# Optimization experiments

Measured on AMD Instinct MI355X. Metric: run time of the kernel, lower is better.

Reference implementation:

```python
import jax, jax.numpy as jnp
import numpy as np

HIDDEN = 2048
NUM_HEADS = 16
HEAD_DIM = HIDDEN // NUM_HEADS  # 128
SCALE = HEAD_DIM ** -0.5


def setup_inputs() -> dict:
    key = jax.random.key(0)
    ks = jax.random.split(key, 5)
    B, S = 2, 2048
    init = HIDDEN ** -0.5  # roughly kaiming-uniform scale for Linear weights
    return {
        "hidden_states": jax.random.normal(ks[0], (B, S, HIDDEN), dtype=jnp.float32),
        "Wq": jax.random.normal(ks[1], (HIDDEN, HIDDEN), dtype=jnp.float32) * init,
        "Wk": jax.random.normal(ks[2], (HIDDEN, HIDDEN), dtype=jnp.float32) * init,
        "Wv": jax.random.normal(ks[3], (HIDDEN, HIDDEN), dtype=jnp.float32) * init,
        "Wo": jax.random.normal(ks[4], (HIDDEN, HIDDEN), dtype=jnp.float32) * init,
    }


def reference(hidden_states, Wq, Wk, Wv, Wo):
    B, S, _ = hidden_states.shape
    # Projections (nn.Linear: x @ W.T; weights stored as [out, in])
    q = (hidden_states @ Wq.T).reshape(B, S, NUM_HEADS, HEAD_DIM).transpose(0, 2, 1, 3)
    k = (hidden_states @ Wk.T).reshape(B, S, NUM_HEADS, HEAD_DIM).transpose(0, 2, 1, 3)
    v = (hidden_states @ Wv.T).reshape(B, S, NUM_HEADS, HEAD_DIM).transpose(0, 2, 1, 3)
    # Full quadratic attention (faithful to the source's explicit materialization)
    scores = jnp.einsum("bhqd,bhkd->bhqk", q, k) * SCALE  # [B,H,S,S]
    probs = jax.nn.softmax(scores, axis=-1)
    attn = jnp.einsum("bhqk,bhkd->bhqd", probs, v)  # [B,H,S,Dh]
    attn = attn.transpose(0, 2, 1, 3).reshape(B, S, HIDDEN)
    return attn @ Wo.T
```

## Files before the change

### kernel.cpp

```cpp
#include <hip/hip_runtime.h>
#include <cstdint>

#define HIDDEN 2048
#define NHEADS 16
#define DH 128
#define BATCH 2
#define SEQ 2048
#define MTOT 4096
#define BH (BATCH * NHEADS)

typedef __attribute__((ext_vector_type(8))) short bf16x8;
typedef __attribute__((ext_vector_type(4))) float f32x4;

static constexpr float QSCALE = (float)(0.08838834764831845 * 1.4426950408889634);

__device__ __forceinline__ unsigned short f2bf(float f) {
  union { float f; uint32_t u; } v; v.f = f;
  uint32_t r = v.u + 0x7FFFu + ((v.u >> 16) & 1u);
  return (unsigned short)(r >> 16);
}
__device__ __forceinline__ uint32_t cvtpk(float lo, float hi) {
  uint32_t r;
  asm("v_cvt_pk_bf16_f32 %0, %1, %2" : "=v"(r) : "v"(lo), "v"(hi));
  return r;
}
__device__ __forceinline__ f32x4 mfma16(bf16x8 a, bf16x8 b, f32x4 c) {
  return __builtin_amdgcn_mfma_f32_16x16x32_bf16(a, b, c, 0, 0, 0);
}

typedef const __attribute__((address_space(1))) unsigned char* gas1_t;
typedef __attribute__((address_space(3))) unsigned char* las3_t;
__device__ __forceinline__ void gll16(const void* g, void* l) {
  __builtin_amdgcn_global_load_lds((gas1_t)g, (las3_t)l, 16, 0, 0);
}

__global__ __launch_bounds__(256) void cast_all(
    const float* __restrict__ X, const float* __restrict__ Wq,
    const float* __restrict__ Wk, const float* __restrict__ Wv,
    const float* __restrict__ Wo, unsigned short* __restrict__ Xb,
    unsigned short* __restrict__ Wqb, unsigned short* __restrict__ Wkb,
    unsigned short* __restrict__ Wvb, unsigned short* __restrict__ Wob) {
  const int n1 = MTOT * HIDDEN;
  const int i = (blockIdx.x * 256 + threadIdx.x) * 4;
  const float* s;
  unsigned short* d;
  int o;
  if (i < n1) {
    s = X; d = Xb; o = i;
  } else {
    const int j = i - n1;
    const int w = j >> 22;
    o = j & ((1 << 22) - 1);
    s = (w == 0) ? Wq : (w == 1) ? Wk : (w == 2) ? Wv : Wo;
    d = (w == 0) ? Wqb : (w == 1) ? Wkb : (w == 2) ? Wvb : Wob;
  }
  float4 f = *(const float4*)&s[o];
  ushort4 u;
  u.x = f2bf(f.x); u.y = f2bf(f.y); u.z = f2bf(f.z); u.w = f2bf(f.w);
  *(ushort4*)&d[o] = u;
}

__global__ __launch_bounds__(256) void gemm_qkv_pipe(
    const unsigned short* __restrict__ A, const unsigned short* __restrict__ Wq,
    const unsigned short* __restrict__ Wk, const unsigned short* __restrict__ Wv,
    unsigned short* __restrict__ Qb, unsigned short* __restrict__ Kb,
    unsigned short* __restrict__ Vb) {
  __shared__ __align__(16) char SM[65536];
  const int tid = threadIdx.x;
  const int lane = tid & 63, wv = tid >> 6;
  const int wr = wv >> 1, wc = wv & 1;
  const int g = lane >> 4, lr = lane & 15;
  const int which = blockIdx.x >> 4;
  const int m0 = blockIdx.y * 128, n0 = (blockIdx.x & 15) * 128;
  const unsigned short* W = (which == 0) ? Wq : (which == 1) ? Wk : Wv;

  const unsigned short* aS[4];
  const unsigned short* bS[4];
#pragma unroll
  for (int j = 0; j < 4; ++j) {
    const int c = j * 256 + tid;
    const int row = c >> 3, cc = (c & 7) ^ (row & 7);
    aS[j] = A + (size_t)(m0 + row) * HIDDEN + cc * 8;
    bS[j] = W + (size_t)(n0 + row) * HIDDEN + cc * 8;
  }

  f32x4 acc[4][4];
#pragma unroll
  for (int i = 0; i < 4; ++i)
#pragma unroll
    for (int j = 0; j < 4; ++j) acc[i][j] = (f32x4){0.f, 0.f, 0.f, 0.f};

#pragma unroll
  for (int j = 0; j < 4; ++j) {
    gll16(aS[j], SM + j * 4096 + wv * 1024);
    gll16(bS[j], SM + 16384 + j * 4096 + wv * 1024);
  }

  const int rx = lr & 7;
  for (int t = 0; t < 32; ++t) {
    const char* slot = SM + (t & 1) * 32768;
    asm volatile("s_waitcnt vmcnt(0)" ::: "memory");
    __builtin_amdgcn_s_barrier();
    if (t + 1 < 32) {
      char* nslot = SM + ((t + 1) & 1) * 32768;
      const size_t ko = (size_t)(t + 1) * 64;
#pragma unroll
      for (int j = 0; j < 4; ++j) {
        gll16(aS[j] + ko, nslot + j * 4096 + wv * 1024);
        gll16(bS[j] + ko, nslot + 16384 + j * 4096 + wv * 1024);
      }
    }
    bf16x8 a0[4], b0[4], a1[4], b1[4];
#pragma unroll
    for (int mi = 0; mi < 4; ++mi) {
      const int row = wr * 64 + mi * 16 + lr;
      a0[mi] = *(const bf16x8*)(slot + row * 128 + ((g ^ rx) * 16));
      a1[mi] = *(const bf16x8*)(slot + row * 128 + (((4 + g) ^ rx) * 16));
    }
#pragma unroll
    for (int ni = 0; ni < 4; ++ni) {
      const int row = wc * 64 + ni * 16 + lr;
      b0[ni] = *(const bf16x8*)(slot + 16384 + row * 128 + ((g ^ rx) * 16));
      b1[ni] = *(const bf16x8*)(slot + 16384 + row * 128 + (((4 + g) ^ rx) * 16));
    }
    __builtin_amdgcn_s_setprio(1);
#pragma unroll
    for (int mi = 0; mi < 4; ++mi)
#pragma unroll
      for (int ni = 0; ni < 4; ++ni)
        acc[mi][ni] = mfma16(a0[mi], b0[ni], acc[mi][ni]);
#pragma unroll
    for (int mi = 0; mi < 4; ++mi)
#pragma unroll
      for (int ni = 0; ni < 4; ++ni)
        acc[mi][ni] = mfma16(a1[mi], b1[ni], acc[mi][ni]);
    __builtin_amdgcn_s_setprio(0);
  }

  const float alpha = (which == 0) ? QSCALE : 1.0f;
  unsigned short* C = (which == 0) ? Qb : (which == 1) ? Kb : Vb;
#pragma unroll
  for (int mi = 0; mi < 4; ++mi)
#pragma unroll
    for (int ni = 0; ni < 4; ++ni)
#pragma unroll
      for (int r = 0; r < 4; ++r) {
        const int row = m0 + wr * 64 + mi * 16 + g * 4 + r;
        const int col = n0 + wc * 64 + ni * 16 + lr;
        const unsigned short v = f2bf(acc[mi][ni][r] * alpha);
        const int b = row >> 11, s = row & (SEQ - 1);
        const int h = col >> 7, d = col & (DH - 1);
        const size_t base = (size_t)(b * NHEADS + h) * SEQ * DH;
        if (which == 0)
          C[base + (size_t)s * DH + d] = v;
        else if (which == 1)
          C[base + (size_t)(s >> 5) * 4096 + (d >> 3) * 256 + (s & 31) * 8 + (d & 7)] = v;
        else
          C[base + (size_t)(s >> 3) * 1024 + d * 8 + (s & 7)] = v;
      }
}

template <int VM, bool PF>
__device__ __forceinline__ void pipe_body(
    int kt, char* SM, const unsigned short* aS0, const unsigned short* aS1,
    const unsigned short* bS0, const unsigned short* bS1,
    const unsigned short* bS2, const unsigned short* bS3, int wv, int wr,
    int wc, int g, int lr, f32x4 (&acc)[4][4]) {
  const char* Ac = SM + (kt % 3) * 49152;
  const char* Bc = Ac + 16384;
  char* slot2 = SM + ((kt + 2) % 3) * 49152;
  const size_t ko = (size_t)(kt + 2) * 64;
  const int rx = lr & 7;
  bf16x8 a0[4], b0[4], a1[4], b1[4];
#pragma unroll
  for (int mi = 0; mi < 4; ++mi)
    a0[mi] = *(const bf16x8*)(Ac + (wr * 64 + mi * 16 + lr) * 128 + ((g ^ rx) * 16));
#pragma unroll
  for (int ni = 0; ni < 4; ++ni)
    b0[ni] = *(const bf16x8*)(Bc + (wc * 64 + ni * 16 + lr) * 128 + ((g ^ rx) * 16));
  if (PF) {
    gll16(aS0 + ko, slot2 + wv * 2048);
    gll16(aS1 + ko, slot2 + wv * 2048 + 1024);
    gll16(bS0 + ko, slot2 + 16384 + wv * 4096);
    gll16(bS1 + ko, slot2 + 16384 + wv * 4096 + 1024);
    gll16(bS2 + ko, slot2 + 16384 + wv * 4096 + 2048);
    gll16(bS3 + ko, slot2 + 16384 + wv * 4096 + 3072);
  }
#pragma unroll
  for (int mi = 0; mi < 4; ++mi)
    a1[mi] = *(const bf16x8*)(Ac + (wr * 64 + mi * 16 + lr) * 128 + (((4 + g) ^ rx) * 16));
#pragma unroll
  for (int ni = 0; ni < 4; ++ni)
    b1[ni] = *(const bf16x8*)(Bc + (wc * 64 + ni * 16 + lr) * 128 + (((4 + g) ^ rx) * 16));
  __builtin_amdgcn_s_setprio(1);
#pragma unroll
  for (int mi = 0; mi < 4; ++mi)
#pragma unroll
    for (int ni = 0; ni < 4; ++ni)
      acc[mi][ni] = mfma16(a0[mi], b0[ni], acc[mi][ni]);
#pragma unroll
  for (int mi = 0; mi < 4; ++mi)
#pragma unroll
    for (int ni = 0; ni < 4; ++ni)
      acc[mi][ni] = mfma16(a1[mi], b1[ni], acc[mi][ni]);
  __builtin_amdgcn_s_setprio(0);
  if (VM == 6) asm volatile("s_waitcnt vmcnt(6)" ::: "memory");
  else if (VM == 0) asm volatile("s_waitcnt vmcnt(0)" ::: "memory");
  if (VM >= 0) __builtin_amdgcn_s_barrier();
}

__global__ __launch_bounds__(512) void gemm_out_pipe(
    const unsigned short* __restrict__ A, const unsigned short* __restrict__ W,
    float* __restrict__ C) {
  __shared__ __align__(16) char SM[147456];
  const int tid = threadIdx.x;
  const int lane = tid & 63, wv = tid >> 6;
  const int wr = wv >> 2, wc = wv & 3;
  const int g = lane >> 4, lr = lane & 15;
  const int m0 = blockIdx.y * 128, n0 = blockIdx.x * 256;

  const int idxA0 = wv * 128 + lane, idxA1 = idxA0 + 64;
  const int rA0 = idxA0 >> 3, cA0 = (idxA0 & 7) ^ (rA0 & 7);
  const int rA1 = idxA1 >> 3, cA1 = (idxA1 & 7) ^ (rA1 & 7);
  const unsigned short* aS0 = A + (size_t)(m0 + rA0) * HIDDEN + cA0 * 8;
  const unsigned short* aS1 = A + (size_t)(m0 + rA1) * HIDDEN + cA1 * 8;
  const int idxB0 = wv * 256 + lane, idxB1 = idxB0 + 64,
            idxB2 = idxB0 + 128, idxB3 = idxB0 + 192;
  const int rB0 = idxB0 >> 3, cB0 = (idxB0 & 7) ^ (rB0 & 7);
  const int rB1 = idxB1 >> 3, cB1 = (idxB1 & 7) ^ (rB1 & 7);
  const int rB2 = idxB2 >> 3, cB2 = (idxB2 & 7) ^ (rB2 & 7);
  const int rB3 = idxB3 >> 3, cB3 = (idxB3 & 7) ^ (rB3 & 7);
  const unsigned short* bS0 = W + (size_t)(n0 + rB0) * HIDDEN + cB0 * 8;
  const unsigned short* bS1 = W + (size_t)(n0 + rB1) * HIDDEN + cB1 * 8;
  const unsigned short* bS2 = W + (size_t)(n0 + rB2) * HIDDEN + cB2 * 8;
  const unsigned short* bS3 = W + (size_t)(n0 + rB3) * HIDDEN + cB3 * 8;

  f32x4 acc[4][4];
#pragma unroll
  for (int i = 0; i < 4; ++i)
#pragma unroll
    for (int j = 0; j < 4; ++j) acc[i][j] = (f32x4){0.f, 0.f, 0.f, 0.f};

#pragma unroll
  for (int tt = 0; tt < 2; ++tt) {
    char* slot = SM + tt * 49152;
    const size_t ko = (size_t)tt * 64;
    gll16(aS0 + ko, slot + wv * 2048);
    gll16(aS1 + ko, slot + wv * 2048 + 1024);
    gll16(bS0 + ko, slot + 16384 + wv * 4096);
    gll16(bS1 + ko, slot + 16384 + wv * 4096 + 1024);
    gll16(bS2 + ko, slot + 16384 + wv * 4096 + 2048);
    gll16(bS3 + ko, slot + 16384 + wv * 4096 + 3072);
  }
  asm volatile("s_waitcnt vmcnt(6)" ::: "memory");
  __builtin_amdgcn_s_barrier();

  for (int kt = 0; kt < 30; ++kt)
    pipe_body<6, true>(kt, SM, aS0, aS1, bS0, bS1, bS2, bS3, wv, wr, wc, g,
                       lr, acc);
  pipe_body<0, false>(30, SM, aS0, aS1, bS0, bS1, bS2, bS3, wv, wr, wc, g,
                      lr, acc);
  pipe_body<-1, false>(31, SM, aS0, aS1, bS0, bS1, bS2, bS3, wv, wr, wc, g,
                       lr, acc);

#pragma unroll
  for (int mi = 0; mi < 4; ++mi)
#pragma unroll
    for (int ni = 0; ni < 4; ++ni)
#pragma unroll
      for (int r = 0; r < 4; ++r) {
        const int row = m0 + wr * 64 + mi * 16 + g * 4 + r;
        const int col = n0 + wc * 64 + ni * 16 + lr;
        C[(size_t)row * HIDDEN + col] = acc[mi][ni][r];
      }
}

__global__ __launch_bounds__(256, 4) void attn_mfma(const unsigned short* __restrict__ Q,
                                                    const unsigned short* __restrict__ K,
                                                    const unsigned short* __restrict__ V,
                                                    unsigned short* __restrict__ Ab) {
  const int bid = blockIdx.x;
  const int bh = bid & 31;
  const int q0 = (bid >> 5) * 64;
  const int tid = threadIdx.x;
  const int wv = tid >> 6, lane = tid & 63;
  const int g = lane >> 4, lr = lane & 15;
  const unsigned short* Qh = Q + (size_t)bh * SEQ * DH;
  const unsigned short* Kh = K + (size_t)bh * SEQ * DH;
  const unsigned short* Vh = V + (size_t)bh * SEQ * DH;

  __shared__ __align__(16) unsigned short Kls[2][4096];
  __shared__ __align__(16) unsigned short Vls[2][4096];
  __shared__ __align__(16) unsigned short Pw[4][16][40];

  bf16x8 qf[4];
#pragma unroll
  for (int kb = 0; kb < 4; ++kb)
    qf[kb] = *(const bf16x8*)&Qh[(size_t)(q0 + wv * 16 + lr) * DH + kb * 32 + g * 8];

  f32x4 acc[8];
#pragma unroll
  for (int dn = 0; dn < 8; ++dn) acc[dn] = (f32x4){0.f, 0.f, 0.f, 0.f};
  float mrun = -1e30f;
  float lrun = 0.f;

#pragma unroll
  for (int j = 0; j < 2; ++j) {
    const int c = j * 256 + tid;
    gll16(Kh + (size_t)c * 8, (char*)&Kls[0][0] + j * 4096 + wv * 1024);
    gll16(Vh + (size_t)c * 8, (char*)&Vls[0][0] + j * 4096 + wv * 1024);
  }

  for (int t = 0; t < 64; ++t) {
    const int cur = t & 1;
    asm volatile("s_waitcnt vmcnt(0)" ::: "memory");
    __builtin_amdgcn_s_barrier();
    if (t + 1 < 64) {
      const unsigned short* Kn = Kh + (size_t)(t + 1) * 4096;
      const unsigned short* Vn = Vh + (size_t)(t + 1) * 4096;
      char* kd = (char*)&Kls[cur ^ 1][0];
      char* vd = (char*)&Vls[cur ^ 1][0];
#pragma unroll
      for (int j = 0; j < 2; ++j) {
        const int c = j * 256 + tid;
        gll16(Kn + (size_t)c * 8, kd + j * 4096 + wv * 1024);
        gll16(Vn + (size_t)c * 8, vd + j * 4096 + wv * 1024);
      }
    }

    const char* Kc = (const char*)&Kls[cur][0];
    const char* Vc = (const char*)&Vls[cur][0];

    f32x4 st0 = (f32x4){0.f, 0.f, 0.f, 0.f};
    f32x4 st1 = (f32x4){0.f, 0.f, 0.f, 0.f};
    __builtin_amdgcn_s_setprio(1);
#pragma unroll
    for (int kb = 0; kb < 4; ++kb) {
      const int cb = (kb * 4 + g) * 32;
      bf16x8 kf0 = *(const bf16x8*)(Kc + (cb + lr) * 16);
      bf16x8 kf1 = *(const bf16x8*)(Kc + (cb + 16 + lr) * 16);
      st0 = mfma16(kf0, qf[kb], st0);
      st1 = mfma16(kf1, qf[kb], st1);
    }
    __builtin_amdgcn_s_setprio(0);
    float mt = fmaxf(fmaxf(fmaxf(st0[0], st0[1]), fmaxf(st0[2], st0[3])),
                     fmaxf(fmaxf(st1[0], st1[1]), fmaxf(st1[2], st1[3])));
    mt = fmaxf(mt, __shfl_xor(mt, 16));
    mt = fmaxf(mt, __shfl_xor(mt, 32));
    if (!__all(mt <= mrun + 8.0f)) {
      const float mnew = fmaxf(mrun, mt);
      const float corr = __builtin_amdgcn_exp2f(mrun - mnew);
      lrun *= corr;
      mrun = mnew;
      const f32x4 cv = (f32x4){__shfl(corr, g * 4 + 0), __shfl(corr, g * 4 + 1),
                               __shfl(corr, g * 4 + 2), __shfl(corr, g * 4 + 3)};
#pragma unroll
      for (int dn = 0; dn < 8; ++dn) acc[dn] *= cv;
    }
    float p[8], ls = 0.f;
#pragma unroll
    for (int r = 0; r < 4; ++r) {
      p[r] = __builtin_amdgcn_exp2f(st0[r] - mrun);
      p[4 + r] = __builtin_amdgcn_exp2f(st1[r] - mrun);
      ls += p[r] + p[4 + r];
    }
    lrun += ls;
    uint2 pk0, pk1;
    pk0.x = cvtpk(p[0], p[1]); pk0.y = cvtpk(p[2], p[3]);
    pk1.x = cvtpk(p[4], p[5]); pk1.y = cvtpk(p[6], p[7]);
    *(uint2*)&Pw[wv][lr][4 * g] = pk0;
    *(uint2*)&Pw[wv][lr][16 + 4 * g] = pk1;
    bf16x8 ap = *(const bf16x8*)&Pw[wv][lr][8 * g];
    __builtin_amdgcn_s_setprio(1);
#pragma unroll
    for (int dn = 0; dn < 8; ++dn) {
      bf16x8 vf = *(const bf16x8*)(Vc + (g * 128 + dn * 16 + lr) * 16);
      acc[dn] = mfma16(ap, vf, acc[dn]);
    }
    __builtin_amdgcn_s_setprio(0);
  }

  const int b = bh >> 4, h = bh & 15;
  lrun += __shfl_xor(lrun, 16);
  lrun += __shfl_xor(lrun, 32);
  const float inv = 1.f / lrun;
  float ir[4];
#pragma unroll
  for (int r = 0; r < 4; ++r) ir[r] = __shfl(inv, g * 4 + r);
#pragma unroll
  for (int dn = 0; dn < 8; ++dn)
#pragma unroll
    for (int r = 0; r < 4; ++r) {
      const int srow = q0 + wv * 16 + g * 4 + r;
      Ab[((size_t)(b * SEQ + srow) * NHEADS + h) * DH + dn * 16 + lr] =
          f2bf(acc[dn][r] * ir[r]);
    }
}

extern "C" void kernel_launch(void* const* d_in, const int* in_sizes, int n_in,
                              void* d_out, int out_size, void* d_ws,
                              size_t ws_size, hipStream_t stream) {
  const float* X  = (const float*)d_in[0];
  const float* Wq = (const float*)d_in[1];
  const float* Wk = (const float*)d_in[2];
  const float* Wv = (const float*)d_in[3];
  const float* Wo = (const float*)d_in[4];
  float* out = (float*)d_out;

  const int n1 = MTOT * HIDDEN;
  const int n2 = HIDDEN * HIDDEN;

  char* p = (char*)d_ws;
  unsigned short* Xb  = (unsigned short*)(p + 0);
  unsigned short* Qb  = (unsigned short*)(p + 16777216);
  unsigned short* Kb  = (unsigned short*)(p + 33554432);
  unsigned short* Vb  = (unsigned short*)(p + 50331648);
  unsigned short* Wqb = (unsigned short*)(p + 67108864);
  unsigned short* Wkb = (unsigned short*)(p + 75497472);
  unsigned short* Wvb = (unsigned short*)(p + 83886080);
  unsigned short* Wob = (unsigned short*)(p + 92274688);
  unsigned short* Ab  = (unsigned short*)(p + 100663296);

  cast_all<<<(n1 + 4 * n2) / 1024, 256, 0, stream>>>(X, Wq, Wk, Wv, Wo, Xb, Wqb,
                                                     Wkb, Wvb, Wob);

  gemm_qkv_pipe<<<dim3(48, MTOT / 128), 256, 0, stream>>>(Xb, Wqb, Wkb, Wvb,
                                                          Qb, Kb, Vb);

  attn_mfma<<<dim3(1024), 256, 0, stream>>>(Qb, Kb, Vb, Ab);

  gemm_out_pipe<<<dim3(HIDDEN / 256, MTOT / 128), 512, 0, stream>>>(Ab, Wob, out);
}
```

Before: 285.6 us.

## Fuse Q/K/V projections into one kernel sharing the A tile with triple buffering

Replaces the per-projection QKV GEMM (48x32 blocks, each loading its own A tile) with a fused kernel where each 512-thread block computes the same 128x128 output tile for Q, K and V together. The A tile is loaded once and reused across the three weight matrices. The K loop now uses 32-wide k steps with a three-slot shared-memory pipeline and partial vmcnt waits instead of a two-slot vmcnt(0) loop. This cuts redundant A traffic and raises per-block work, but uses 96KB of LDS and 96 accumulator floats per thread. That may lower occupancy and leaves only 512 blocks.

New measurement: 272.0 us. -4.8%, faster.

```diff
diff --git a/kernel.cpp b/kernel.cpp
--- a/kernel.cpp
+++ b/kernel.cpp
@@ -60,103 +60,112 @@
   *(ushort4*)&d[o] = u;
 }
 
-__global__ __launch_bounds__(256) void gemm_qkv_pipe(
+template <int VM, bool PF>
+__device__ __forceinline__ void qkv3_body(
+    int t, char* SM, const unsigned short* aS, const unsigned short* bSq,
+    const unsigned short* bSk, const unsigned short* bSv, int wv, int wr,
+    int wc, int g, int lr, f32x4 (&accQ)[4][2], f32x4 (&accK)[4][2],
+    f32x4 (&accV)[4][2]) {
+  const char* slot = SM + (t % 3) * 32768;
+  char* slot2 = SM + ((t + 2) % 3) * 32768;
+  const size_t ko = (size_t)(t + 2) * 32;
+  const int coff = (g ^ ((lr >> 1) & 3)) * 16;
+  bf16x8 a[4], bq[2], bk[2], bv[2];
+#pragma unroll
+  for (int mi = 0; mi < 4; ++mi)
+    a[mi] = *(const bf16x8*)(slot + (wr * 64 + mi * 16 + lr) * 64 + coff);
+#pragma unroll
+  for (int ni = 0; ni < 2; ++ni) {
+    const int brow = (wc * 32 + ni * 16 + lr) * 64 + coff;
+    bq[ni] = *(const bf16x8*)(slot + 8192 + brow);
+    bk[ni] = *(const bf16x8*)(slot + 16384 + brow);
+    bv[ni] = *(const bf16x8*)(slot + 24576 + brow);
+  }
+  if (PF) {
+    gll16(aS + ko, slot2 + wv * 1024);
+    gll16(bSq + ko, slot2 + 8192 + wv * 1024);
+    gll16(bSk + ko, slot2 + 16384 + wv * 1024);
+    gll16(bSv + ko, slot2 + 24576 + wv * 1024);
+  }
+  __builtin_amdgcn_s_setprio(1);
+#pragma unroll
+  for (int mi = 0; mi < 4; ++mi)
+#pragma unroll
+    for (int ni = 0; ni < 2; ++ni) {
+      accQ[mi][ni] = mfma16(a[mi], bq[ni], accQ[mi][ni]);
+      accK[mi][ni] = mfma16(a[mi], bk[ni], accK[mi][ni]);
+      accV[mi][ni] = mfma16(a[mi], bv[ni], accV[mi][ni]);
+    }
+  __builtin_amdgcn_s_setprio(0);
+  if (VM == 4) asm volatile("s_waitcnt vmcnt(4)" ::: "memory");
+  else if (VM == 0) asm volatile("s_waitcnt vmcnt(0)" ::: "memory");
+  if (VM >= 0) __builtin_amdgcn_s_barrier();
+}
+
+__global__ __launch_bounds__(512) void gemm_qkv_fused(
     const unsigned short* __restrict__ A, const unsigned short* __restrict__ Wq,
     const unsigned short* __restrict__ Wk, const unsigned short* __restrict__ Wv,
     unsigned short* __restrict__ Qb, unsigned short* __restrict__ Kb,
     unsigned short* __restrict__ Vb) {
-  __shared__ __align__(16) char SM[65536];
+  __shared__ __align__(16) char SM[98304];
   const int tid = threadIdx.x;
   const int lane = tid & 63, wv = tid >> 6;
-  const int wr = wv >> 1, wc = wv & 1;
+  const int wr = wv >> 2, wc = wv & 3;
   const int g = lane >> 4, lr = lane & 15;
-  const int which = blockIdx.x >> 4;
-  const int m0 = blockIdx.y * 128, n0 = (blockIdx.x & 15) * 128;
-  const unsigned short* W = (which == 0) ? Wq : (which == 1) ? Wk : Wv;
-
-  const unsigned short* aS[4];
-  const unsigned short* bS[4];
-#pragma unroll
-  for (int j = 0; j < 4; ++j) {
-    const int c = j * 256 + tid;
-    const int row = c >> 3, cc = (c & 7) ^ (row & 7);
-    aS[j] = A + (size_t)(m0 + row) * HIDDEN + cc * 8;
-    bS[j] = W + (size_t)(n0 + row) * HIDDEN + cc * 8;
-  }
-
-  f32x4 acc[4][4];
+  const int m0 = blockIdx.y * 128, n0 = blockIdx.x * 128;
+
+  const int row0 = tid >> 2, j0 = (tid & 3) ^ ((row0 >> 1) & 3);
+  const unsigned short* aS  = A  + (size_t)(m0 + row0) * HIDDEN + j0 * 8;
+  const unsigned short* bSq = Wq + (size_t)(n0 + row0) * HIDDEN + j0 * 8;
+  const unsigned short* bSk = Wk + (size_t)(n0 + row0) * HIDDEN + j0 * 8;
+  const unsigned short* bSv = Wv + (size_t)(n0 + row0) * HIDDEN + j0 * 8;
+
+  f32x4 accQ[4][2], accK[4][2], accV[4][2];
 #pragma unroll
   for (int i = 0; i < 4; ++i)
 #pragma unroll
-    for (int j = 0; j < 4; ++j) acc[i][j] = (f32x4){0.f, 0.f, 0.f, 0.f};
-
-#pragma unroll
-  for (int j = 0; j < 4; ++j) {
-    gll16(aS[j], SM + j * 4096 + wv * 1024);
-    gll16(bS[j], SM + 16384 + j * 4096 + wv * 1024);
-  }
-
-  const int rx = lr & 7;
-  for (int t = 0; t < 32; ++t) {
-    const char* slot = SM + (t & 1) * 32768;
-    asm volatile("s_waitcnt vmcnt(0)" ::: "memory");
-    __builtin_amdgcn_s_barrier();
-    if (t + 1 < 32) {
-      char* nslot = SM + ((t + 1) & 1) * 32768;
-      const size_t ko = (size_t)(t + 1) * 64;
-#pragma unroll
-      for (int j = 0; j < 4; ++j) {
-        gll16(aS[j] + ko, nslot + j * 4096 + wv * 1024);
-        gll16(bS[j] + ko, nslot + 16384 + j * 4096 + wv * 1024);
-      }
-    }
-    bf16x8 a0[4], b0[4], a1[4], b1[4];
-#pragma unroll
-    for (int mi = 0; mi < 4; ++mi) {
-      const int row = wr * 64 + mi * 16 + lr;
-      a0[mi] = *(const bf16x8*)(slot + row * 128 + ((g ^ rx) * 16));
-      a1[mi] = *(const bf16x8*)(slot + row * 128 + (((4 + g) ^ rx) * 16));
-    }
-#pragma unroll
-    for (int ni = 0; ni < 4; ++ni) {
-      const int row = wc * 64 + ni * 16 + lr;
-      b0[ni] = *(const bf16x8*)(slot + 16384 + row * 128 + ((g ^ rx) * 16));
-      b1[ni] = *(const bf16x8*)(slot + 16384 + row * 128 + (((4 + g) ^ rx) * 16));
-    }
-    __builtin_amdgcn_s_setprio(1);
-#pragma unroll
-    for (int mi = 0; mi < 4; ++mi)
-#pragma unroll
-      for (int ni = 0; ni < 4; ++ni)
-        acc[mi][ni] = mfma16(a0[mi], b0[ni], acc[mi][ni]);
-#pragma unroll
-    for (int mi = 0; mi < 4; ++mi)
-#pragma unroll
-      for (int ni = 0; ni < 4; ++ni)
-        acc[mi][ni] = mfma16(a1[mi], b1[ni], acc[mi][ni]);
-    __builtin_amdgcn_s_setprio(0);
-  }
-
-  const float alpha = (which == 0) ? QSCALE : 1.0f;
-  unsigned short* C = (which == 0) ? Qb : (which == 1) ? Kb : Vb;
-#pragma unroll
-  for (int mi = 0; mi < 4; ++mi)
-#pragma unroll
-    for (int ni = 0; ni < 4; ++ni)
+    for (int j = 0; j < 2; ++j) {
+      accQ[i][j] = (f32x4){0.f, 0.f, 0.f, 0.f};
+      accK[i][j] = (f32x4){0.f, 0.f, 0.f, 0.f};
+      accV[i][j] = (f32x4){0.f, 0.f, 0.f, 0.f};
+    }
+
+#pragma unroll
+  for (int tt = 0; tt < 2; ++tt) {
+    char* slot = SM + tt * 32768;
+    const size_t ko = (size_t)tt * 32;
+    gll16(aS + ko, slot + wv * 1024);
+    gll16(bSq + ko, slot + 8192 + wv * 1024);
+    gll16(bSk + ko, slot + 16384 + wv * 1024);
+    gll16(bSv + ko, slot + 24576 + wv * 1024);
+  }
+  asm volatile("s_waitcnt vmcnt(4)" ::: "memory");
+  __builtin_amdgcn_s_barrier();
+
+  for (int t = 0; t < 62; ++t)
+    qkv3_body<4, true>(t, SM, aS, bSq, bSk, bSv, wv, wr, wc, g, lr,
+                       accQ, accK, accV);
+  qkv3_body<0, false>(62, SM, aS, bSq, bSk, bSv, wv, wr, wc, g, lr,
+                      accQ, accK, accV);
+  qkv3_body<-1, false>(63, SM, aS, bSq, bSk, bSv, wv, wr, wc, g, lr,
+                       accQ, accK, accV);
+
+#pragma unroll
+  for (int mi = 0; mi < 4; ++mi)
+#pragma unroll
+    for (int ni = 0; ni < 2; ++ni)
 #pragma unroll
       for (int r = 0; r < 4; ++r) {
         const int row = m0 + wr * 64 + mi * 16 + g * 4 + r;
-        const int col = n0 + wc * 64 + ni * 16 + lr;
-        const unsigned short v = f2bf(acc[mi][ni][r] * alpha);
+        const int col = n0 + wc * 32 + ni * 16 + lr;
         const int b = row >> 11, s = row & (SEQ - 1);
         const int h = col >> 7, d = col & (DH - 1);
         const size_t base = (size_t)(b * NHEADS + h) * SEQ * DH;
-        if (which == 0)
-          C[base + (size_t)s * DH + d] = v;
-        else if (which == 1)
-          C[base + (size_t)(s >> 5) * 4096 + (d >> 3) * 256 + (s & 31) * 8 + (d & 7)] = v;
-        else
-          C[base + (size_t)(s >> 3) * 1024 + d * 8 + (s & 7)] = v;
+        Qb[base + (size_t)s * DH + d] = f2bf(accQ[mi][ni][r] * QSCALE);
+        Kb[base + (size_t)(s >> 5) * 4096 + (d >> 3) * 256 + (s & 31) * 8 + (d & 7)] =
+            f2bf(accK[mi][ni][r]);
+        Vb[base + (size_t)(s >> 3) * 1024 + d * 8 + (s & 7)] =
+            f2bf(accV[mi][ni][r]);
       }
 }
 
@@ -424,8 +433,8 @@
   cast_all<<<(n1 + 4 * n2) / 1024, 256, 0, stream>>>(X, Wq, Wk, Wv, Wo, Xb, Wqb,
                                                      Wkb, Wvb, Wob);
 
-  gemm_qkv_pipe<<<dim3(48, MTOT / 128), 256, 0, stream>>>(Xb, Wqb, Wkb, Wvb,
-                                                          Qb, Kb, Vb);
+  gemm_qkv_fused<<<dim3(HIDDEN / 128, MTOT / 128), 512, 0, stream>>>(
+      Xb, Wqb, Wkb, Wvb, Qb, Kb, Vb);
 
   attn_mfma<<<dim3(1024), 256, 0, stream>>>(Qb, Kb, Vb, Ab);
 
```
